# Kernel optimization log

Hardware: AMD Instinct MI355X
Metric: run time of the kernel (lower is better)

Reference implementation:

```python
import jax, jax.numpy as jnp
import numpy as np

BS = 4
EMBED = 256
HEADS = 8
LEVELS = 4
POINTS = 4
HD = EMBED // HEADS  # 32
SHAPES = np.array([[96, 96], [48, 48], [24, 24], [12, 12]], dtype=np.int64)
LQ = int((SHAPES[:, 0] * SHAPES[:, 1]).sum())  # 12240


def _offset_bias():
    # faithful to MSDeformableAttention._reset_parameters grid init
    thetas = np.arange(HEADS, dtype=np.float32) * (2.0 * np.pi / HEADS)
    g = np.stack([np.cos(thetas), np.sin(thetas)], -1)
    g = g / np.abs(g).max(-1, keepdims=True)
    g = np.tile(g.reshape(HEADS, 1, 1, 2), (1, LEVELS, POINTS, 1))
    g = g * np.arange(1, POINTS + 1, dtype=np.float32).reshape(1, 1, -1, 1)
    return jnp.asarray(g.reshape(-1), dtype=jnp.float32)


def setup_inputs() -> dict:
    key = jax.random.key(0)
    ks = jax.random.split(key, 8)
    tp = HEADS * LEVELS * POINTS
    d = {}
    d["query"] = jax.random.normal(ks[0], (BS, LQ, EMBED), jnp.float32)
    d["reference_points"] = jax.random.uniform(ks[1], (BS, LQ, LEVELS, 2), jnp.float32)
    d["value"] = jax.random.normal(ks[2], (BS, LQ, EMBED), jnp.float32)
    d["value_spatial_shapes"] = SHAPES  # static numpy, int
    d["W_off"] = jax.random.normal(ks[3], (EMBED, tp * 2), jnp.float32) * 0.01
    d["b_off"] = _offset_bias()
    d["W_attn"] = jax.random.normal(ks[4], (EMBED, tp), jnp.float32) * 0.02
    d["b_attn"] = jnp.zeros((tp,), jnp.float32)
    d["W_val"] = jax.random.normal(ks[5], (EMBED, EMBED), jnp.float32) * (1.0 / np.sqrt(EMBED).astype(np.float32))
    d["b_val"] = jnp.zeros((EMBED,), jnp.float32)
    d["W_out"] = jax.random.normal(ks[6], (EMBED, EMBED), jnp.float32) * (1.0 / np.sqrt(EMBED).astype(np.float32))
    d["b_out"] = jnp.zeros((EMBED,), jnp.float32)
    return d


def _bilinear_sample(img, grid):
    # img: [B,H,W,C]; grid: [B,Q,P,2] in [-1,1] (x,y)
    # matches F.grid_sample(mode='bilinear', padding_mode='zeros', align_corners=False)
    B, H, W, C = img.shape
    gx = (grid[..., 0] + 1.0) * (W * 0.5) - 0.5
    gy = (grid[..., 1] + 1.0) * (H * 0.5) - 0.5
    x0 = jnp.floor(gx)
    y0 = jnp.floor(gy)
    wx = gx - x0
    wy = gy - y0
    x0i = x0.astype(jnp.int32)
    y0i = y0.astype(jnp.int32)
    x1i = x0i + 1
    y1i = y0i + 1
    flat = img.reshape(B, H * W, C)

    def corner(xi, yi, w):
        valid = (xi >= 0) & (xi < W) & (yi >= 0) & (yi < H)
        idx = jnp.clip(yi, 0, H - 1) * W + jnp.clip(xi, 0, W - 1)
        v = jnp.take_along_axis(flat, idx.reshape(B, -1, 1), axis=1)
        v = v.reshape(idx.shape + (C,))
        return v * (w * valid)[..., None]

    return (corner(x0i, y0i, (1.0 - wx) * (1.0 - wy))
            + corner(x1i, y0i, wx * (1.0 - wy))
            + corner(x0i, y1i, (1.0 - wx) * wy)
            + corner(x1i, y1i, wx * wy))


def reference(query, reference_points, value, value_spatial_shapes,
              W_off, b_off, W_attn, b_attn, W_val, b_val, W_out, b_out):
    shapes = np.asarray(value_spatial_shapes)  # static [L,2] (H,W)
    bs, Lq, _ = query.shape
    v = (value @ W_val + b_val).reshape(bs, -1, HEADS, HD)  # [bs,Lv,H,hd]
    off = (query @ W_off + b_off).reshape(bs, Lq, HEADS, LEVELS, POINTS, 2)
    aw = jax.nn.softmax((query @ W_attn + b_attn).reshape(bs, Lq, HEADS, LEVELS * POINTS), axis=-1)
    aw = aw.reshape(bs, Lq, HEADS, LEVELS, POINTS)
    # normalizer is (W,H) per level
    norm = jnp.asarray(shapes[:, ::-1].copy(), jnp.float32).reshape(1, 1, 1, LEVELS, 1, 2)
    loc = reference_points[:, :, None, :, None, :] + off / norm
    grids = 2.0 * loc - 1.0  # [bs,Lq,H,L,P,2]

    acc = jnp.zeros((bs * HEADS, Lq, HD), query.dtype)
    start = 0
    for lvl in range(LEVELS):
        h, w = int(shapes[lvl, 0]), int(shapes[lvl, 1])
        v_l = v[:, start:start + h * w].reshape(bs, h, w, HEADS, HD)
        v_l = v_l.transpose(0, 3, 1, 2, 4).reshape(bs * HEADS, h, w, HD)
        g_l = grids[:, :, :, lvl].transpose(0, 2, 1, 3, 4).reshape(bs * HEADS, Lq, POINTS, 2)
        s_l = _bilinear_sample(v_l, g_l)  # [bs*H, Lq, P, hd]
        w_l = aw[:, :, :, lvl].transpose(0, 2, 1, 3).reshape(bs * HEADS, Lq, POINTS)
        acc = acc + jnp.einsum('bqpc,bqp->bqc', s_l, w_l)
        start += h * w

    out = acc.reshape(bs, HEADS, Lq, HD).transpose(0, 2, 1, 3).reshape(bs, Lq, EMBED)
    return out @ W_out + b_out
```

## Files before the change

### kernel.cpp

```cpp
#include <hip/hip_runtime.h>
#include <hip/hip_bf16.h>

static constexpr int BS     = 4;
static constexpr int EMBED  = 256;
static constexpr int HEADS  = 8;
static constexpr int LEVELS = 4;
static constexpr int POINTS = 4;
static constexpr int HD     = 32;
static constexpr int LQ     = 12240;
static constexpr int NROW   = BS * LQ;
static constexpr int LVL_W[4]  = {96, 48, 24, 12};
static constexpr int LVL_H[4]  = {96, 48, 24, 12};
static constexpr int LVL_ST[4] = {0, 9216, 11520, 12096};

typedef __attribute__((ext_vector_type(8))) short short8;
typedef __attribute__((ext_vector_type(4))) float f32x4;
typedef _Float16 h2 __attribute__((ext_vector_type(2)));

__device__ __forceinline__ unsigned short f2bf(float f) {
    unsigned int u = __float_as_uint(f);
    unsigned int r = (u + 0x7FFFu + ((u >> 16) & 1u)) >> 16;
    return (unsigned short)r;
}

__device__ __forceinline__ unsigned int pkh(float a, float b) {
    const unsigned int ua = __builtin_bit_cast(unsigned short, (_Float16)a);
    const unsigned int ub = __builtin_bit_cast(unsigned short, (_Float16)b);
    return ua | (ub << 16);
}

__device__ __forceinline__ float dot2(float acc, unsigned int v, unsigned int w) {
#if __has_builtin(__builtin_amdgcn_fdot2)
    return __builtin_amdgcn_fdot2(__builtin_bit_cast(h2, v),
                                  __builtin_bit_cast(h2, w), acc, false);
#else
    asm("v_dot2_f32_f16 %0, %1, %2, %0" : "+v"(acc) : "v"(v), "v"(w));
    return acc;
#endif
}

__global__ __launch_bounds__(256) void prep_weights(
    const float* __restrict__ W_off, const float* __restrict__ W_attn,
    const float* __restrict__ W_val, const float* __restrict__ W_out,
    unsigned short* __restrict__ WT_oa, unsigned short* __restrict__ WT_val,
    unsigned short* __restrict__ WT_out)
{
    const int gid = blockIdx.x * 256 + threadIdx.x;
    const int k = gid & 255;
    const int n = gid >> 8;
    if (n < 384) {
        const float v = (n < 256) ? W_off[k * 256 + n] : W_attn[k * 128 + (n - 256)];
        WT_oa[n * 256 + k] = f2bf(v);
    } else if (n < 640) {
        const int nn = n - 384;
        WT_val[nn * 256 + k] = f2bf(W_val[k * 256 + nn]);
    } else {
        const int nn = n - 640;
        WT_out[nn * 256 + k] = f2bf(W_out[k * 256 + nn]);
    }
}

template <int NCH, bool A_BF16, int OMODE>
__global__ __launch_bounds__(256, 3) void gemm_persist(
    const void* __restrict__ Av, const unsigned short* __restrict__ Wt,
    const float* __restrict__ bias0, const float* __restrict__ bias1, int nsplit,
    void* __restrict__ Cv)
{
    constexpr int K = 256;
    __shared__ __align__(16) unsigned short Af[64][264];
    __shared__ __align__(16) unsigned short Bs[128][40];

    const int tid = threadIdx.x;
    const int m0 = blockIdx.x * 64;
    const int w  = tid >> 6;
    const int l  = tid & 63;
    const int lm = l & 15;
    const int lq = l >> 4;

    const int sr = tid >> 2;
    const int kg = (tid & 3) * 8;

    if (A_BF16) {
        const unsigned short* A = (const unsigned short*)Av;
        #pragma unroll
        for (int k0 = 0; k0 < K; k0 += 32)
            *(short8*)&Af[sr][k0 + kg] = *(const short8*)&A[(size_t)(m0 + sr) * K + k0 + kg];
    } else {
        const float* A = (const float*)Av;
        #pragma unroll
        for (int k0 = 0; k0 < K; k0 += 32) {
            const float* ap = &A[(size_t)(m0 + sr) * K + k0 + kg];
            const float4 a0 = *(const float4*)ap;
            const float4 a1 = *(const float4*)(ap + 4);
            uint4 pk;
            pk.x = (unsigned int)f2bf(a0.x) | ((unsigned int)f2bf(a0.y) << 16);
            pk.y = (unsigned int)f2bf(a0.z) | ((unsigned int)f2bf(a0.w) << 16);
            pk.z = (unsigned int)f2bf(a1.x) | ((unsigned int)f2bf(a1.y) << 16);
            pk.w = (unsigned int)f2bf(a1.z) | ((unsigned int)f2bf(a1.w) << 16);
            *(uint4*)&Af[sr][k0 + kg] = pk;
        }
    }

    short8 pb[2];
    auto gloadB = [&](int n0, int k0) {
        #pragma unroll
        for (int i = 0; i < 2; ++i) {
            const int slot = tid + i * 256;
            const int n  = slot >> 2;
            const int kk = (slot & 3) * 8;
            pb[i] = *(const short8*)&Wt[(size_t)(n0 + n) * K + k0 + kk];
        }
    };
    gloadB(0, 0);
    __syncthreads();

    #pragma unroll
    for (int ch = 0; ch < NCH; ++ch) {
        const int n0 = ch * 128;
        f32x4 acc[4][2];
        #pragma unroll
        for (int rg = 0; rg < 4; ++rg) {
            acc[rg][0] = (f32x4){0.f, 0.f, 0.f, 0.f};
            acc[rg][1] = (f32x4){0.f, 0.f, 0.f, 0.f};
        }

        #pragma unroll 2
        for (int k0 = 0; k0 < K; k0 += 32) {
            #pragma unroll
            for (int i = 0; i < 2; ++i) {
                const int slot = tid + i * 256;
                const int n  = slot >> 2;
                const int kk = (slot & 3) * 8;
                *(short8*)&Bs[n][kk] = pb[i];
            }
            __syncthreads();

            if (k0 + 32 < K)       gloadB(n0, k0 + 32);
            else if (ch + 1 < NCH) gloadB(n0 + 128, 0);

            short8 af[4];
            #pragma unroll
            for (int rg = 0; rg < 4; ++rg)
                af[rg] = *(const short8*)&Af[rg * 16 + lm][k0 + lq * 8];
            #pragma unroll
            for (int nt = 0; nt < 2; ++nt) {
                const short8 bf = *(const short8*)&Bs[(w * 2 + nt) * 16 + lm][lq * 8];
                #pragma unroll
                for (int rg = 0; rg < 4; ++rg)
                    acc[rg][nt] = __builtin_amdgcn_mfma_f32_16x16x32_bf16(af[rg], bf, acc[rg][nt], 0, 0, 0);
            }
            __syncthreads();
        }

        #pragma unroll
        for (int nt = 0; nt < 2; ++nt) {
            const int col = n0 + (w * 2 + nt) * 16 + lm;
            const float b = (col < nsplit) ? bias0[col] : bias1[col - nsplit];
            #pragma unroll
            for (int rg = 0; rg < 4; ++rg)
                #pragma unroll
                for (int r = 0; r < 4; ++r) {
                    const int row = m0 + rg * 16 + lq * 4 + r;
                    const float v = acc[rg][nt][r] + b;
                    if (OMODE == 0)
                        ((unsigned short*)Cv)[(size_t)row * 256 + col] =
                            __builtin_bit_cast(unsigned short, (_Float16)v);
                    else if (OMODE == 1)
                        ((float*)Cv)[(size_t)row * 384 + col] = v;
                    else
                        ((float*)Cv)[(size_t)row * 256 + col] = v;
                }
        }
    }
}

__global__ __launch_bounds__(256, 4) void sample_kernel(
    const unsigned short* __restrict__ V,
    const float* __restrict__ OA,
    const float* __restrict__ refp,
    unsigned short* __restrict__ ACC)
{
    __shared__ __align__(16) unsigned int pr_o[512][4];
    __shared__ __align__(16) unsigned int pr_w[512][2];

    const int tid = threadIdx.x;

    const unsigned bx = blockIdx.x;
    const int xcd  = bx & 7;
    const int slot = bx >> 3;
    const int batch = xcd >> 1;
    const int wb   = slot * 2 + (xcd & 1);
    const int row0 = batch * LQ + wb * 4;

    {
        float4* dstb = (float4*)pr_o;
        const float4* src = (const float4*)(OA + (size_t)row0 * 384);
        {
            const int i = tid, rr = i / 96, ww = i % 96;
            dstb[rr * 96 + (ww ^ ((ww >> 3) & 7))] = src[i];
        }
        if (tid < 128) {
            const int i = tid + 256, rr = i / 96, ww = i % 96;
            dstb[rr * 96 + (ww ^ ((ww >> 3) & 7))] = src[i];
        }
        __syncthreads();

        const int g = tid & 31;
        const int r = g >> 3;
        const int h = g & 7;
        const int L = tid >> 5;
        const float* stg = (const float*)pr_o + r * 384;

        auto swzf4 = [](int f4) { return f4 ^ ((f4 >> 3) & 7); };

        const int f4l0 = 64 + ((h * 16 + L) >> 2);
        const int f4l1 = 64 + ((h * 16 + L + 8) >> 2);
        const float lg0 = stg[swzf4(f4l0) * 4 + (L & 3)];
        const float lg1 = stg[swzf4(f4l1) * 4 + (L & 3)];

        float* smax = (float*)pr_w;
        float* ssum = smax + 264;
        smax[L * 33 + g] = fmaxf(lg0, lg1);
        __syncthreads();
        float m = smax[g];
        #pragma unroll
        for (int k = 1; k < 8; ++k) m = fmaxf(m, smax[k * 33 + g]);
        const float e0 = __expf(lg0 - m);
        const float e1 = __expf(lg1 - m);
        ssum[L * 33 + g] = e0 + e1;
        __syncthreads();
        float sden = ssum[g];
        #pragma unroll
        for (int k = 1; k < 8; ++k) sden += ssum[k * 33 + g];
        const float inv = 1.0f / sden;

        uint4 ostash[2];
        uint2 wstash[2];
        int   sidx[2];
        #pragma unroll
        for (int ss = 0; ss < 2; ++ss) {
            const int lp  = L + ss * 8;
            const int s   = lp * 32 + g;
            const int lvl = lp >> 2;
            const int Wl = LVL_W[lvl], Hl = LVL_H[lvl], st = LVL_ST[lvl];

            const int f4c = h * 8 + (lp >> 1);
            const float2 oxy = *(const float2*)&stg[swzf4(f4c) * 4 + (lp & 1) * 2];
            const float2 rxy = *(const float2*)&refp[(size_t)(row0 + r) * 8 + lvl * 2];
            const float wgt = (ss ? e1 : e0) * inv;

            const float gx = (rxy.x + oxy.x / (float)Wl) * (float)Wl - 0.5f;
            const float gy = (rxy.y + oxy.y / (float)Hl) * (float)Hl - 0.5f;

            const float fx = floorf(gx), fy = floorf(gy);
            const float wx = gx - fx,    wy = gy - fy;
            const int x0 = (int)fx, y0 = (int)fy;
            const int x1 = x0 + 1,  y1 = y0 + 1;

            const bool bx0 = ((unsigned)x0 < (unsigned)Wl);
            const bool bx1 = ((unsigned)x1 < (unsigned)Wl);
            const bool by0 = ((unsigned)y0 < (unsigned)Hl);
            const bool by1 = ((unsigned)y1 < (unsigned)Hl);
            const float w00 = (bx0 && by0) ? (1.f - wx) * (1.f - wy) * wgt : 0.f;
            const float w10 = (bx1 && by0) ? wx * (1.f - wy) * wgt : 0.f;
            const float w01 = (bx0 && by1) ? (1.f - wx) * wy * wgt : 0.f;
            const float w11 = (bx1 && by1) ? wx * wy * wgt : 0.f;

            const int cx0 = min(max(x0, 0), Wl - 1);
            const int cx1 = min(max(x1, 0), Wl - 1);
            const int cy0 = min(max(y0, 0), Hl - 1);
            const int cy1 = min(max(y1, 0), Hl - 1);

            uint4 o;
            o.x = (unsigned int)(st + cy0 * Wl + cx0) * 512u;
            o.y = (unsigned int)(st + cy0 * Wl + cx1) * 512u;
            o.z = (unsigned int)(st + cy1 * Wl + cx0) * 512u;
            o.w = (unsigned int)(st + cy1 * Wl + cx1) * 512u;
            ostash[ss] = o;
            wstash[ss] = make_uint2(pkh(w00, w10), pkh(w01, w11));
            sidx[ss] = s;
        }
        __syncthreads();
        *(uint4*)&pr_o[sidx[0]][0] = ostash[0];
        *(uint4*)&pr_o[sidx[1]][0] = ostash[1];
        *(uint2*)&pr_w[sidx[0]][0] = wstash[0];
        *(uint2*)&pr_w[sidx[1]][0] = wstash[1];
    }
    __syncthreads();

    const int w    = tid >> 6;
    const int l    = tid & 63;
    const int half = l >> 5;
    const int head = (l >> 2) & 7;
    const int c16  = (l & 3) * 16;

    const int row  = __builtin_amdgcn_readfirstlane(row0 + w);
    const char* vrow = (const char*)V + (size_t)batch * ((size_t)LQ * 512);
    const unsigned int lane_byte = (unsigned int)(head * 64 + c16);
    const int sid0 = half * 256 + w * 8 + head;

    constexpr unsigned SEL_LO = 0x01000504u;
    constexpr unsigned SEL_HI = 0x03020706u;

    uint4 ofs[4];
    uint2 wpk[4];
    uint4 dat[3][4];
    float acc[8];
    #pragma unroll
    for (int i = 0; i < 8; ++i) acc[i] = 0.f;

    auto ldpr = [&](int j, int sl) {
        ofs[sl] = *(const uint4*)&pr_o[sid0 + j * 32][0];
        wpk[sl] = *(const uint2*)&pr_w[sid0 + j * 32][0];
    };
    auto ldglb = [&](int osl, int dsl) {
        const uint4 o = ofs[osl];
        dat[dsl][0] = *(const uint4*)(vrow + (lane_byte + o.x));
        dat[dsl][1] = *(const uint4*)(vrow + (lane_byte + o.y));
        dat[dsl][2] = *(const uint4*)(vrow + (lane_byte + o.z));
        dat[dsl][3] = *(const uint4*)(vrow + (lane_byte + o.w));
    };
    auto cpair = [&](const uint4& d0, const uint4& d1, unsigned wp) {
        acc[0] = dot2(acc[0], __builtin_amdgcn_perm(d0.x, d1.x, SEL_LO), wp);
        acc[1] = dot2(acc[1], __builtin_amdgcn_perm(d0.x, d1.x, SEL_HI), wp);
        acc[2] = dot2(acc[2], __builtin_amdgcn_perm(d0.y, d1.y, SEL_LO), wp);
        acc[3] = dot2(acc[3], __builtin_amdgcn_perm(d0.y, d1.y, SEL_HI), wp);
        acc[4] = dot2(acc[4], __builtin_amdgcn_perm(d0.z, d1.z, SEL_LO), wp);
        acc[5] = dot2(acc[5], __builtin_amdgcn_perm(d0.z, d1.z, SEL_HI), wp);
        acc[6] = dot2(acc[6], __builtin_amdgcn_perm(d0.w, d1.w, SEL_LO), wp);
        acc[7] = dot2(acc[7], __builtin_amdgcn_perm(d0.w, d1.w, SEL_HI), wp);
    };
    auto consume = [&](int dsl, int wsl) {
        cpair(dat[dsl][0], dat[dsl][1], wpk[wsl].x);
        cpair(dat[dsl][2], dat[dsl][3], wpk[wsl].y);
    };

    ldpr(0, 0); ldpr(1, 1); ldpr(2, 2);
    ldglb(0, 0); ldglb(1, 1);
    #pragma unroll
    for (int j = 0; j < 8; ++j) {
        if (j + 2 < 8) ldglb((j + 2) & 3, (j + 2) % 3);
        if (j + 3 < 8) ldpr(j + 3, (j + 3) & 3);
        consume(j % 3, j & 3);
    }

    #pragma unroll
    for (int i = 0; i < 8; ++i) acc[i] += __shfl_xor(acc[i], 32);

    if (half == 0) {
        uint4 o;
        o.x = (unsigned int)f2bf(acc[0]) | ((unsigned int)f2bf(acc[1]) << 16);
        o.y = (unsigned int)f2bf(acc[2]) | ((unsigned int)f2bf(acc[3]) << 16);
        o.z = (unsigned int)f2bf(acc[4]) | ((unsigned int)f2bf(acc[5]) << 16);
        o.w = (unsigned int)f2bf(acc[6]) | ((unsigned int)f2bf(acc[7]) << 16);
        *(uint4*)((char*)(ACC + (size_t)row * EMBED) + head * 64 + c16) = o;
    }
}

extern "C" void kernel_launch(void* const* d_in, const int* in_sizes, int n_in,
                              void* d_out, int out_size, void* d_ws, size_t ws_size,
                              hipStream_t stream) {
    const float* query  = (const float*)d_in[0];
    const float* refp   = (const float*)d_in[1];
    const float* value  = (const float*)d_in[2];
    const float* W_off  = (const float*)d_in[4];
    const float* b_off  = (const float*)d_in[5];
    const float* W_attn = (const float*)d_in[6];
    const float* b_attn = (const float*)d_in[7];
    const float* W_val  = (const float*)d_in[8];
    const float* b_val  = (const float*)d_in[9];
    const float* W_out  = (const float*)d_in[10];
    const float* b_out  = (const float*)d_in[11];
    float* out = (float*)d_out;

    unsigned short* WT_oa  = (unsigned short*)d_ws;
    unsigned short* WT_val = WT_oa  + 384 * 256;
    unsigned short* WT_out = WT_val + 256 * 256;
    unsigned short* V      = WT_out + 256 * 256;
    float*          OA     = (float*)(V + (size_t)NROW * EMBED);
    unsigned short* ACCb   = (unsigned short*)(OA + (size_t)NROW * 384);

    dim3 blk(256);

    prep_weights<<<896, blk, 0, stream>>>(W_off, W_attn, W_val, W_out,
                                          WT_oa, WT_val, WT_out);
    gemm_persist<2, false, 0><<<NROW / 64, blk, 0, stream>>>(
        value, WT_val, b_val, b_val, 256, V);
    gemm_persist<3, false, 1><<<NROW / 64, blk, 0, stream>>>(
        query, WT_oa, b_off, b_attn, 256, OA);
    sample_kernel<<<NROW / 4, blk, 0, stream>>>(V, OA, refp, ACCb);
    gemm_persist<2, true, 2><<<NROW / 64, blk, 0, stream>>>(
        ACCb, WT_out, b_out, b_out, 256, out);
}
```

Baseline: 320.1 us.

## Merge value and offset GEMMs into one launch, widen B tile K-step

Fuses the value-projection and offset/attention-projection GEMMs into a single kernel launch, using a block-index split so both run concurrently across the GPU. Both GEMM kernels now stage 64-wide K slices of B in shared memory instead of 32, which halves the number of barrier pairs per chunk at the cost of more registers and LDS. The sample kernel's shared-memory swizzle also XORs in the row index to cut bank conflicts when reading per-row logits. Occupancy hints switch to amdgpu_waves_per_eu.

New measurement: 322.8 us. About the same (+0.8%).

```diff
diff --git a/kernel.cpp b/kernel.cpp
--- a/kernel.cpp
+++ b/kernel.cpp
@@ -60,15 +60,122 @@
     }
 }
 
-template <int NCH, bool A_BF16, int OMODE>
-__global__ __launch_bounds__(256, 3) void gemm_persist(
-    const void* __restrict__ Av, const unsigned short* __restrict__ Wt,
-    const float* __restrict__ bias0, const float* __restrict__ bias1, int nsplit,
-    void* __restrict__ Cv)
+__global__ __launch_bounds__(256) __attribute__((amdgpu_waves_per_eu(3, 3)))
+void gemm_vo(
+    const float* __restrict__ Aval, const float* __restrict__ Aqry,
+    const unsigned short* __restrict__ Wval, const unsigned short* __restrict__ Woa,
+    const float* __restrict__ bval, const float* __restrict__ boff,
+    const float* __restrict__ battn,
+    unsigned short* __restrict__ Vout, float* __restrict__ OAout)
 {
-    constexpr int K = 256;
     __shared__ __align__(16) unsigned short Af[64][264];
-    __shared__ __align__(16) unsigned short Bs[128][40];
+    __shared__ __align__(16) unsigned short Bs[128][72];
+
+    const int x    = blockIdx.x;
+    const bool isV = (x < 765);
+    const int  m0  = (isV ? x : x - 765) * 64;
+    const float* A = isV ? Aval : Aqry;
+    const unsigned short* Wt = isV ? Wval : Woa;
+    const int nch  = isV ? 2 : 3;
+
+    const int tid = threadIdx.x;
+    const int w  = tid >> 6;
+    const int l  = tid & 63;
+    const int lm = l & 15;
+    const int lq = l >> 4;
+    const int sr = tid >> 2;
+    const int kg = (tid & 3) * 8;
+
+    #pragma unroll
+    for (int k0 = 0; k0 < 256; k0 += 32) {
+        const float* ap = &A[(size_t)(m0 + sr) * 256 + k0 + kg];
+        const float4 a0 = *(const float4*)ap;
+        const float4 a1 = *(const float4*)(ap + 4);
+        uint4 pk;
+        pk.x = (unsigned int)f2bf(a0.x) | ((unsigned int)f2bf(a0.y) << 16);
+        pk.y = (unsigned int)f2bf(a0.z) | ((unsigned int)f2bf(a0.w) << 16);
+        pk.z = (unsigned int)f2bf(a1.x) | ((unsigned int)f2bf(a1.y) << 16);
+        pk.w = (unsigned int)f2bf(a1.z) | ((unsigned int)f2bf(a1.w) << 16);
+        *(uint4*)&Af[sr][k0 + kg] = pk;
+    }
+
+    short8 pb[4];
+    auto gloadB = [&](int n0, int k0) {
+        #pragma unroll
+        for (int i = 0; i < 4; ++i) {
+            const int slot = tid + i * 256;
+            const int n  = slot >> 3;
+            const int kk = (slot & 7) * 8;
+            pb[i] = *(const short8*)&Wt[(size_t)(n0 + n) * 256 + k0 + kk];
+        }
+    };
+    gloadB(0, 0);
+    __syncthreads();
+
+    for (int ch = 0; ch < nch; ++ch) {
+        const int n0 = ch * 128;
+        f32x4 acc[4][2];
+        #pragma unroll
+        for (int rg = 0; rg < 4; ++rg) {
+            acc[rg][0] = (f32x4){0.f, 0.f, 0.f, 0.f};
+            acc[rg][1] = (f32x4){0.f, 0.f, 0.f, 0.f};
+        }
+
+        #pragma unroll
+        for (int k0 = 0; k0 < 256; k0 += 64) {
+            #pragma unroll
+            for (int i = 0; i < 4; ++i) {
+                const int slot = tid + i * 256;
+                *(short8*)&Bs[slot >> 3][(slot & 7) * 8] = pb[i];
+            }
+            __syncthreads();
+
+            if (k0 + 64 < 256)      gloadB(n0, k0 + 64);
+            else if (ch + 1 < nch)  gloadB(n0 + 128, 0);
+
+            #pragma unroll
+            for (int ks = 0; ks < 64; ks += 32) {
+                short8 af[4];
+                #pragma unroll
+                for (int rg = 0; rg < 4; ++rg)
+                    af[rg] = *(const short8*)&Af[rg * 16 + lm][k0 + ks + lq * 8];
+                #pragma unroll
+                for (int nt = 0; nt < 2; ++nt) {
+                    const short8 bf = *(const short8*)&Bs[(w * 2 + nt) * 16 + lm][ks + lq * 8];
+                    #pragma unroll
+                    for (int rg = 0; rg < 4; ++rg)
+                        acc[rg][nt] = __builtin_amdgcn_mfma_f32_16x16x32_bf16(af[rg], bf, acc[rg][nt], 0, 0, 0);
+                }
+            }
+            __syncthreads();
+        }
+
+        #pragma unroll
+        for (int nt = 0; nt < 2; ++nt) {
+            const int col = n0 + (w * 2 + nt) * 16 + lm;
+            const float b = isV ? bval[col]
+                                : ((col < 256) ? boff[col] : battn[col - 256]);
+            #pragma unroll
+            for (int rg = 0; rg < 4; ++rg)
+                #pragma unroll
+                for (int r = 0; r < 4; ++r) {
+                    const int row = m0 + rg * 16 + lq * 4 + r;
+                    const float v = acc[rg][nt][r] + b;
+                    if (isV) Vout[(size_t)row * 256 + col] =
+                                 __builtin_bit_cast(unsigned short, (_Float16)v);
+                    else     OAout[(size_t)row * 384 + col] = v;
+                }
+        }
+    }
+}
+
+__global__ __launch_bounds__(256) __attribute__((amdgpu_waves_per_eu(3, 3)))
+void gemm_out(
+    const unsigned short* __restrict__ A, const unsigned short* __restrict__ Wt,
+    const float* __restrict__ bias, float* __restrict__ Cv)
+{
+    __shared__ __align__(16) unsigned short Af[64][264];
+    __shared__ __align__(16) unsigned short Bs[128][72];
 
     const int tid = threadIdx.x;
     const int m0 = blockIdx.x * 64;
@@ -76,46 +183,28 @@
     const int l  = tid & 63;
     const int lm = l & 15;
     const int lq = l >> 4;
-
     const int sr = tid >> 2;
     const int kg = (tid & 3) * 8;
 
-    if (A_BF16) {
-        const unsigned short* A = (const unsigned short*)Av;
-        #pragma unroll
-        for (int k0 = 0; k0 < K; k0 += 32)
-            *(short8*)&Af[sr][k0 + kg] = *(const short8*)&A[(size_t)(m0 + sr) * K + k0 + kg];
-    } else {
-        const float* A = (const float*)Av;
-        #pragma unroll
-        for (int k0 = 0; k0 < K; k0 += 32) {
-            const float* ap = &A[(size_t)(m0 + sr) * K + k0 + kg];
-            const float4 a0 = *(const float4*)ap;
-            const float4 a1 = *(const float4*)(ap + 4);
-            uint4 pk;
-            pk.x = (unsigned int)f2bf(a0.x) | ((unsigned int)f2bf(a0.y) << 16);
-            pk.y = (unsigned int)f2bf(a0.z) | ((unsigned int)f2bf(a0.w) << 16);
-            pk.z = (unsigned int)f2bf(a1.x) | ((unsigned int)f2bf(a1.y) << 16);
-            pk.w = (unsigned int)f2bf(a1.z) | ((unsigned int)f2bf(a1.w) << 16);
-            *(uint4*)&Af[sr][k0 + kg] = pk;
-        }
-    }
-
-    short8 pb[2];
+    #pragma unroll
+    for (int k0 = 0; k0 < 256; k0 += 32)
+        *(short8*)&Af[sr][k0 + kg] = *(const short8*)&A[(size_t)(m0 + sr) * 256 + k0 + kg];
+
+    short8 pb[4];
     auto gloadB = [&](int n0, int k0) {
         #pragma unroll
-        for (int i = 0; i < 2; ++i) {
+        for (int i = 0; i < 4; ++i) {
             const int slot = tid + i * 256;
-            const int n  = slot >> 2;
-            const int kk = (slot & 3) * 8;
-            pb[i] = *(const short8*)&Wt[(size_t)(n0 + n) * K + k0 + kk];
+            const int n  = slot >> 3;
+            const int kk = (slot & 7) * 8;
+            pb[i] = *(const short8*)&Wt[(size_t)(n0 + n) * 256 + k0 + kk];
         }
     };
     gloadB(0, 0);
     __syncthreads();
 
     #pragma unroll
-    for (int ch = 0; ch < NCH; ++ch) {
+    for (int ch = 0; ch < 2; ++ch) {
         const int n0 = ch * 128;
         f32x4 acc[4][2];
         #pragma unroll
@@ -124,30 +213,31 @@
             acc[rg][1] = (f32x4){0.f, 0.f, 0.f, 0.f};
         }
 
-        #pragma unroll 2
-        for (int k0 = 0; k0 < K; k0 += 32) {
-            #pragma unroll
-            for (int i = 0; i < 2; ++i) {
+        #pragma unroll
+        for (int k0 = 0; k0 < 256; k0 += 64) {
+            #pragma unroll
+            for (int i = 0; i < 4; ++i) {
                 const int slot = tid + i * 256;
-                const int n  = slot >> 2;
-                const int kk = (slot & 3) * 8;
-                *(short8*)&Bs[n][kk] = pb[i];
+                *(short8*)&Bs[slot >> 3][(slot & 7) * 8] = pb[i];
             }
             __syncthreads();
 
-            if (k0 + 32 < K)       gloadB(n0, k0 + 32);
-            else if (ch + 1 < NCH) gloadB(n0 + 128, 0);
-
-            short8 af[4];
-            #pragma unroll
-            for (int rg = 0; rg < 4; ++rg)
-                af[rg] = *(const short8*)&Af[rg * 16 + lm][k0 + lq * 8];
-            #pragma unroll
-            for (int nt = 0; nt < 2; ++nt) {
-                const short8 bf = *(const short8*)&Bs[(w * 2 + nt) * 16 + lm][lq * 8];
+            if (k0 + 64 < 256)  gloadB(n0, k0 + 64);
+            else if (ch == 0)   gloadB(128, 0);
+
+            #pragma unroll
+            for (int ks = 0; ks < 64; ks += 32) {
+                short8 af[4];
                 #pragma unroll
                 for (int rg = 0; rg < 4; ++rg)
-                    acc[rg][nt] = __builtin_amdgcn_mfma_f32_16x16x32_bf16(af[rg], bf, acc[rg][nt], 0, 0, 0);
+                    af[rg] = *(const short8*)&Af[rg * 16 + lm][k0 + ks + lq * 8];
+                #pragma unroll
+                for (int nt = 0; nt < 2; ++nt) {
+                    const short8 bf = *(const short8*)&Bs[(w * 2 + nt) * 16 + lm][ks + lq * 8];
+                    #pragma unroll
+                    for (int rg = 0; rg < 4; ++rg)
+                        acc[rg][nt] = __builtin_amdgcn_mfma_f32_16x16x32_bf16(af[rg], bf, acc[rg][nt], 0, 0, 0);
+                }
             }
             __syncthreads();
         }
@@ -155,26 +245,20 @@
         #pragma unroll
         for (int nt = 0; nt < 2; ++nt) {
             const int col = n0 + (w * 2 + nt) * 16 + lm;
-            const float b = (col < nsplit) ? bias0[col] : bias1[col - nsplit];
+            const float b = bias[col];
             #pragma unroll
             for (int rg = 0; rg < 4; ++rg)
                 #pragma unroll
                 for (int r = 0; r < 4; ++r) {
                     const int row = m0 + rg * 16 + lq * 4 + r;
-                    const float v = acc[rg][nt][r] + b;
-                    if (OMODE == 0)
-                        ((unsigned short*)Cv)[(size_t)row * 256 + col] =
-                            __builtin_bit_cast(unsigned short, (_Float16)v);
-                    else if (OMODE == 1)
-                        ((float*)Cv)[(size_t)row * 384 + col] = v;
-                    else
-                        ((float*)Cv)[(size_t)row * 256 + col] = v;
+                    Cv[(size_t)row * 256 + col] = acc[rg][nt][r] + b;
                 }
         }
     }
 }
 
-__global__ __launch_bounds__(256, 4) void sample_kernel(
+__global__ __launch_bounds__(256) __attribute__((amdgpu_waves_per_eu(4, 4)))
+void sample_kernel(
     const unsigned short* __restrict__ V,
     const float* __restrict__ OA,
     const float* __restrict__ refp,
@@ -197,11 +281,11 @@
         const float4* src = (const float4*)(OA + (size_t)row0 * 384);
         {
             const int i = tid, rr = i / 96, ww = i % 96;
-            dstb[rr * 96 + (ww ^ ((ww >> 3) & 7))] = src[i];
+            dstb[rr * 96 + (ww ^ ((ww >> 3) & 7) ^ rr)] = src[i];
         }
         if (tid < 128) {
             const int i = tid + 256, rr = i / 96, ww = i % 96;
-            dstb[rr * 96 + (ww ^ ((ww >> 3) & 7))] = src[i];
+            dstb[rr * 96 + (ww ^ ((ww >> 3) & 7) ^ rr)] = src[i];
         }
         __syncthreads();
 
@@ -211,7 +295,7 @@
         const int L = tid >> 5;
         const float* stg = (const float*)pr_o + r * 384;
 
-        auto swzf4 = [](int f4) { return f4 ^ ((f4 >> 3) & 7); };
+        auto swzf4 = [&](int f4) { return f4 ^ ((f4 >> 3) & 7) ^ r; };
 
         const int f4l0 = 64 + ((h * 16 + L) >> 2);
         const int f4l1 = 64 + ((h * 16 + L + 8) >> 2);
@@ -384,11 +468,8 @@
 
     prep_weights<<<896, blk, 0, stream>>>(W_off, W_attn, W_val, W_out,
                                           WT_oa, WT_val, WT_out);
-    gemm_persist<2, false, 0><<<NROW / 64, blk, 0, stream>>>(
-        value, WT_val, b_val, b_val, 256, V);
-    gemm_persist<3, false, 1><<<NROW / 64, blk, 0, stream>>>(
-        query, WT_oa, b_off, b_attn, 256, OA);
+    gemm_vo<<<1530, blk, 0, stream>>>(
+        value, query, WT_val, WT_oa, b_val, b_off, b_attn, V, OA);
     sample_kernel<<<NROW / 4, blk, 0, stream>>>(V, OA, refp, ACCb);
-    gemm_persist<2, true, 2><<<NROW / 64, blk, 0, stream>>>(
-        ACCb, WT_out, b_out, b_out, 256, out);
-}
+    gemm_out<<<NROW / 64, blk, 0, stream>>>(ACCb, WT_out, b_out, out);
+}
```
